# Kernel optimization log

Hardware: AMD Instinct MI355X
Metric: run time of the kernel (lower is better)

The kernel has to match this reference:

```python
import jax, jax.numpy as jnp
import numpy as np

B, SEQ, DIM = 4, 8192, 512
G = 32              # group_size: number of outer chunks (per source rearrange 'b (g n) d')
QK = 128            # query_key_dim
HD = QK // 4        # head_dim = 32 (used for softmax scale)
HEAD_D = 2 * HD     # per-head feature dim = 64 (h=2 heads over QK)
HID = DIM           # expansion_factor = 1.0
EPS = 1e-5


def _shift_seq(t):
    # F.pad(t, (0,0,1,-1)): prepend one zero row along axis=-2, drop last row
    pad = [(0, 0)] * (t.ndim - 2) + [(1, 0), (0, 0)]
    return jnp.pad(t, pad)[..., :-1, :]


def setup_inputs() -> dict:
    key = jax.random.key(0)
    ks = jax.random.split(key, 8)
    s = 0.02
    return {
        "x": jax.random.normal(ks[0], (B, SEQ, DIM), jnp.float32),
        "ln_g": jnp.ones((DIM,), jnp.float32),
        "ln_b": jnp.zeros((DIM,), jnp.float32),
        "w_qk": jax.random.normal(ks[1], (DIM, QK), jnp.float32) * s,
        "g4": jax.random.normal(ks[2], (4, QK), jnp.float32) * s,   # qk_offset_scale.gamma
        "b4": jnp.zeros((4, QK), jnp.float32),                       # qk_offset_scale.beta
        "g2": jax.random.normal(ks[3], (2, QK), jnp.float32) * s,   # shift_one_offset_scale.gamma
        "b2": jnp.zeros((2, QK), jnp.float32),
        "w_hidden": jax.random.normal(ks[4], (DIM, 2 * HID), jnp.float32) * s,
        "w_gate": jax.random.normal(ks[5], (DIM, HID), jnp.float32) * s,
        "w_out": jax.random.normal(ks[6], (5 * HID, DIM), jnp.float32) * s,
    }


def reference(x, ln_g, ln_b, w_qk, g4, b4, g2, b2, w_hidden, w_gate, w_out):
    b, seq, dim = x.shape
    n = seq // G  # tokens per chunk; seq chosen as multiple of G so padding = 0

    # LayerNorm
    mu = jnp.mean(x, axis=-1, keepdims=True)
    var = jnp.var(x, axis=-1, keepdims=True)
    xs = (x - mu) * jax.lax.rsqrt(var + EPS) * ln_g + ln_b

    # token shift of first half of channels (shift_tokens=True)
    half = dim // 2
    xs = jnp.concatenate([_shift_seq(xs[..., :half]), xs[..., half:]], axis=-1)

    qk = xs @ w_qk                                  # [b, seq, QK]
    qk_g = qk.reshape(b, G, n, QK)                  # 'b (g n) d -> b g n d', g outer
    qk_mean = qk_g.mean(axis=2)                     # [b, G, QK]

    # OffsetScale(heads=4) on per-chunk mean -> q_offset, k_offset, q_scale, k_scale
    offs = qk_mean[:, :, None, :] * g4 + b4         # [b, G, 4, QK]
    q_off, k_off, q_sc, k_sc = (offs[:, :, i, :] for i in range(4))

    q = qk_g * q_sc[:, :, None, :] + q_off[:, :, None, :]   # [b, G, n, QK]
    k = qk_g * k_sc[:, :, None, :] + k_off[:, :, None, :]

    # shift-by-one variants within each chunk, re-scaled + shift-one offsets
    q_s_off = qk_mean * g2[0] + b2[0]               # [b, G, QK]
    k_s_off = qk_mean * g2[1] + b2[1]
    qs = _shift_seq(q) * q_sc[:, :, None, :] + q_s_off[:, :, None, :]
    ks_ = _shift_seq(k) * k_sc[:, :, None, :] + k_s_off[:, :, None, :]

    def heads(t):  # [b,G,n,QK] -> [b,G,2,n,HEAD_D]
        return t.reshape(b, G, n, 2, HEAD_D).transpose(0, 1, 3, 2, 4)

    q_all = jnp.concatenate([heads(q), heads(qs)], axis=2)   # [b,G,4,n,64]
    k_all = jnp.concatenate([heads(k), heads(ks_)], axis=2)

    hg = xs @ w_hidden                              # [b, seq, 2*HID]
    hidden, gate = hg[..., :HID], hg[..., HID:]
    hidden_g = hidden.reshape(b, G, n, HID)

    sim = jnp.einsum('bghid,bghjd->bghij', q_all, k_all) * (HD ** -0.5)
    neg = -jnp.finfo(sim.dtype).max
    causal = jnp.triu(jnp.ones((n, n), dtype=bool), 1)  # applied unconditionally in source
    sim = jnp.where(causal, neg, sim)
    attn = jax.nn.softmax(sim, axis=-1)             # dropout=0 (eval)

    out = jnp.einsum('bghij,bgje->bghie', attn, hidden_g)   # [b,G,4,n,HID]
    gate_g = gate.reshape(b, G, n, HID)
    out = jax.nn.silu(out) * gate_g[:, :, None, :, :]
    out = out.transpose(0, 1, 3, 2, 4).reshape(b, seq, 4 * HID)  # 'b g h n e -> b (g n) (h e)'

    residual = jnp.concatenate([hidden, out], axis=-1)       # [b, seq, 5*HID]
    out = residual @ w_out                                   # [b, seq, dim]
    out = out * jax.nn.silu(xs @ w_gate)
    return out + xs
```

## Files before the change

### kernel.cpp

```cpp
#include <hip/hip_runtime.h>
#include <hip/hip_bf16.h>
#include <math.h>

#define BB 4
#define SEQ 8192
#define DIM 512
#define GG 32
#define NPG 256
#define QKD 128
#define HIDD 512

typedef unsigned short u16;
typedef unsigned int u32;

using s16x8 = __attribute__((ext_vector_type(8))) short;
using f32x4 = __attribute__((ext_vector_type(4))) float;

__device__ __forceinline__ float bf2f(u16 u) { return __uint_as_float(((u32)u) << 16); }
__device__ __forceinline__ u16 f2bf(float f) {
  u32 b = __float_as_uint(f);
  return (u16)((b + 0x7FFFu + ((b >> 16) & 1u)) >> 16);
}
__device__ __forceinline__ float silu_f(float x) { return x / (1.f + expf(-x)); }
__device__ __forceinline__ float4 fma4(float4 a, float4 b, float4 c) {
  return make_float4(a.x*b.x+c.x, a.y*b.y+c.y, a.z*b.z+c.z, a.w*b.w+c.w);
}
#define LD4(p, off) (*(const float4*)((p) + (off)))

__device__ __forceinline__ s16x8 aff8(s16x8 v, float4 s0, float4 s1, float4 o0, float4 o1) {
  union U { s16x8 x; u16 u[8]; };
  U in; in.x = v; U r;
  r.u[0] = f2bf(bf2f(in.u[0]) * s0.x + o0.x);
  r.u[1] = f2bf(bf2f(in.u[1]) * s0.y + o0.y);
  r.u[2] = f2bf(bf2f(in.u[2]) * s0.z + o0.z);
  r.u[3] = f2bf(bf2f(in.u[3]) * s0.w + o0.w);
  r.u[4] = f2bf(bf2f(in.u[4]) * s1.x + o1.x);
  r.u[5] = f2bf(bf2f(in.u[5]) * s1.y + o1.y);
  r.u[6] = f2bf(bf2f(in.u[6]) * s1.z + o1.z);
  r.u[7] = f2bf(bf2f(in.u[7]) * s1.w + o1.w);
  return r.x;
}
__device__ __forceinline__ s16x8 aff8s(s16x8 p, bool nz, float4 s0, float4 s1,
                                       float4 o0, float4 o1, float4 t0, float4 t1) {
  union U { s16x8 x; u16 u[8]; };
  U in; in.x = p; U r;
  float v;
  v = nz ? (bf2f(in.u[0]) * s0.x + o0.x) : 0.f; r.u[0] = f2bf(v * s0.x + t0.x);
  v = nz ? (bf2f(in.u[1]) * s0.y + o0.y) : 0.f; r.u[1] = f2bf(v * s0.y + t0.y);
  v = nz ? (bf2f(in.u[2]) * s0.z + o0.z) : 0.f; r.u[2] = f2bf(v * s0.z + t0.z);
  v = nz ? (bf2f(in.u[3]) * s0.w + o0.w) : 0.f; r.u[3] = f2bf(v * s0.w + t0.w);
  v = nz ? (bf2f(in.u[4]) * s1.x + o1.x) : 0.f; r.u[4] = f2bf(v * s1.x + t1.x);
  v = nz ? (bf2f(in.u[5]) * s1.y + o1.y) : 0.f; r.u[5] = f2bf(v * s1.y + t1.y);
  v = nz ? (bf2f(in.u[6]) * s1.z + o1.z) : 0.f; r.u[6] = f2bf(v * s1.z + t1.z);
  v = nz ? (bf2f(in.u[7]) * s1.w + o1.w) : 0.f; r.u[7] = f2bf(v * s1.w + t1.w);
  return r.x;
}

__global__ __launch_bounds__(256) void k_ln(const float* __restrict__ x,
    const float* __restrict__ lg, const float* __restrict__ lb, float* __restrict__ xs) {
  const int row = blockIdx.x;
  const int s = row & (SEQ - 1);
  const int t = threadIdx.x;
  const float* xr = x + (size_t)row * DIM;
  float v0 = xr[t], v1 = xr[t + 256];
  float sum = v0 + v1, sq = v0 * v0 + v1 * v1;
  #pragma unroll
  for (int o = 32; o; o >>= 1) { sum += __shfl_down(sum, o); sq += __shfl_down(sq, o); }
  __shared__ float sm[8];
  const int w = t >> 6;
  if ((t & 63) == 0) { sm[w] = sum; sm[4 + w] = sq; }
  __syncthreads();
  if (t == 0) {
    float S = sm[0] + sm[1] + sm[2] + sm[3];
    float Q = sm[4] + sm[5] + sm[6] + sm[7];
    float mu = S * (1.f / DIM);
    float var = Q * (1.f / DIM) - mu * mu;
    sm[0] = mu; sm[4] = rsqrtf(var + 1e-5f);
  }
  __syncthreads();
  const float mu = sm[0], rs = sm[4];
  float y0 = (v0 - mu) * rs * lg[t] + lb[t];
  float y1 = (v1 - mu) * rs * lg[t + 256] + lb[t + 256];
  xs[(size_t)row * DIM + t + 256] = y1;
  if (s + 1 < SEQ) xs[(size_t)(row + 1) * DIM + t] = y0;
  if (s == 0) xs[(size_t)row * DIM + t] = 0.f;
}

__global__ __launch_bounds__(256) void k_trw(const float* __restrict__ src, u16* __restrict__ dst,
    int N, int dstLD, int rowOff) {
  __shared__ u16 T[64][66];
  const int t = threadIdx.x;
  const int k0 = blockIdx.x * 64, n0 = blockIdx.y * 64;
  #pragma unroll
  for (int i = 0; i < 16; ++i) {
    int idx = t + 256 * i;
    int r = idx >> 6, c = idx & 63;
    T[c][r] = f2bf(src[(size_t)(k0 + r) * N + n0 + c]);
  }
  __syncthreads();
  #pragma unroll
  for (int i = 0; i < 16; ++i) {
    int idx = t + 256 * i;
    int r = idx >> 6, c = idx & 63;
    dst[(size_t)(rowOff + n0 + r) * dstLD + k0 + c] = T[r][c];
  }
}

__global__ __launch_bounds__(256) void k_trh(const u16* __restrict__ hidt, u16* __restrict__ hidr) {
  __shared__ u16 T[64][66];
  const int t = threadIdx.x;
  const int j0 = blockIdx.x * 64;
  const int e0 = blockIdx.y * 64;
  const int bg = blockIdx.z;
  #pragma unroll
  for (int i = 0; i < 16; ++i) {
    int idx = t + 256 * i; int r = idx >> 6, c = idx & 63;
    T[c][r] = hidt[((size_t)bg * 512 + e0 + r) * 256 + j0 + c];
  }
  __syncthreads();
  #pragma unroll
  for (int i = 0; i < 16; ++i) {
    int idx = t + 256 * i; int r = idx >> 6, c = idx & 63;
    hidr[((size_t)bg * 256 + j0 + r) * 512 + e0 + c] = T[r][c];
  }
}

__global__ __launch_bounds__(256, 2) void k_gemm1m(const float* __restrict__ xs,
    const u16* __restrict__ w1t, u16* __restrict__ qk, u16* __restrict__ hidt,
    u16* __restrict__ gate, u16* __restrict__ xg) {
  __shared__ u16 As[128][72];
  __shared__ u16 Bs[128][72];
  const int t = threadIdx.x;
  const int m0 = blockIdx.x * 128, n0 = blockIdx.y * 128;
  const int w = t >> 6, l = t & 63, lr = l & 15, lq = l >> 4;
  const int wr = (w >> 1) * 64, wc = (w & 1) * 64;
  const int sr = t >> 3;
  const int sk = (t & 7) * 8;
  f32x4 acc[4][4];
  #pragma unroll
  for (int i = 0; i < 4; ++i)
    #pragma unroll
    for (int j = 0; j < 4; ++j) acc[i][j] = (f32x4){0.f, 0.f, 0.f, 0.f};
  for (int k0 = 0; k0 < 512; k0 += 64) {
    s16x8 aS[4], bS[4];
    #pragma unroll
    for (int it = 0; it < 4; ++it) {
      const float* ap = xs + (size_t)(m0 + sr + it * 32) * 512 + k0 + sk;
      float4 f0 = *(const float4*)ap;
      float4 f1 = *(const float4*)(ap + 4);
      s16x8 v;
      v[0] = (short)f2bf(f0.x); v[1] = (short)f2bf(f0.y); v[2] = (short)f2bf(f0.z); v[3] = (short)f2bf(f0.w);
      v[4] = (short)f2bf(f1.x); v[5] = (short)f2bf(f1.y); v[6] = (short)f2bf(f1.z); v[7] = (short)f2bf(f1.w);
      aS[it] = v;
      bS[it] = *(const s16x8*)(w1t + (size_t)(n0 + sr + it * 32) * 512 + k0 + sk);
    }
    __syncthreads();
    #pragma unroll
    for (int it = 0; it < 4; ++it) {
      *(s16x8*)&As[sr + it * 32][sk] = aS[it];
      *(s16x8*)&Bs[sr + it * 32][sk] = bS[it];
    }
    __syncthreads();
    #pragma unroll
    for (int kk = 0; kk < 64; kk += 32) {
      s16x8 af[4], bf[4];
      #pragma unroll
      for (int fi = 0; fi < 4; ++fi) af[fi] = *(const s16x8*)&As[wr + fi * 16 + lr][kk + 8 * lq];
      #pragma unroll
      for (int fj = 0; fj < 4; ++fj) bf[fj] = *(const s16x8*)&Bs[wc + fj * 16 + lr][kk + 8 * lq];
      #pragma unroll
      for (int fi = 0; fi < 4; ++fi)
        #pragma unroll
        for (int fj = 0; fj < 4; ++fj)
          acc[fi][fj] = __builtin_amdgcn_mfma_f32_16x16x32_bf16(af[fi], bf[fj], acc[fi][fj], 0, 0, 0);
    }
  }
  if (n0 == 0) {
    #pragma unroll
    for (int fi = 0; fi < 4; ++fi)
      #pragma unroll
      for (int fj = 0; fj < 4; ++fj) {
        const int n = wc + fj * 16 + lr;
        const int mb = m0 + wr + fi * 16 + lq * 4;
        #pragma unroll
        for (int r = 0; r < 4; ++r)
          qk[(size_t)(mb + r) * QKD + n] = f2bf(acc[fi][fj][r]);
      }
  } else if (n0 < 640) {
    const int bg = m0 >> 8;
    #pragma unroll
    for (int fi = 0; fi < 4; ++fi)
      #pragma unroll
      for (int fj = 0; fj < 4; ++fj) {
        const int e = n0 - 128 + wc + fj * 16 + lr;
        const int j0 = (m0 & 255) + wr + fi * 16 + lq * 4;
        ushort4 pk;
        pk.x = f2bf(acc[fi][fj][0]); pk.y = f2bf(acc[fi][fj][1]);
        pk.z = f2bf(acc[fi][fj][2]); pk.w = f2bf(acc[fi][fj][3]);
        *(ushort4*)(hidt + ((size_t)bg * 512 + e) * 256 + j0) = pk;
      }
  } else if (n0 < 1152) {
    #pragma unroll
    for (int fi = 0; fi < 4; ++fi)
      #pragma unroll
      for (int fj = 0; fj < 4; ++fj) {
        const int n = n0 - 640 + wc + fj * 16 + lr;
        const int mb = m0 + wr + fi * 16 + lq * 4;
        #pragma unroll
        for (int r = 0; r < 4; ++r)
          gate[(size_t)(mb + r) * HIDD + n] = f2bf(acc[fi][fj][r]);
      }
  } else {
    #pragma unroll
    for (int fi = 0; fi < 4; ++fi)
      #pragma unroll
      for (int fj = 0; fj < 4; ++fj) {
        const int n = n0 - 1152 + wc + fj * 16 + lr;
        const int mb = m0 + wr + fi * 16 + lq * 4;
        #pragma unroll
        for (int r = 0; r < 4; ++r)
          xg[(size_t)(mb + r) * HIDD + n] = f2bf(silu_f(acc[fi][fj][r]));
      }
  }
}

__global__ __launch_bounds__(128) void k_qkmean(const u16* __restrict__ qk, float* __restrict__ qm) {
  const int bg = blockIdx.x;
  const int c = threadIdx.x;
  const u16* p = qk + (size_t)bg * NPG * QKD + c;
  float s = 0.f;
  for (int i = 0; i < NPG; ++i) s += bf2f(p[(size_t)i * QKD]);
  qm[(size_t)bg * QKD + c] = s * (1.f / NPG);
}

__global__ __launch_bounds__(256, 4) void k_attn(const u16* __restrict__ qk,
    const float* __restrict__ qm, const float* __restrict__ g4, const float* __restrict__ b4,
    const float* __restrict__ g2, const float* __restrict__ b2,
    const u16* __restrict__ hidt, const u16* __restrict__ gate, u16* __restrict__ out4) {
  __shared__ u16 Vs[64][264];
  const int t = threadIdx.x;
  const int l = t & 63;
  const int h = t >> 6;
  const int blk = blockIdx.x;
  const int iw = 15 - (blk & 15);
  const int bg = blk >> 4;
  const size_t grpRow = (size_t)bg * NPG;
  const int cbase = (h & 1) << 6;
  const int lr = l & 15, lq = l >> 4;
  const int i0 = iw * 16, ntmax = iw, jtmax = iw >> 1;
  const int irow = i0 + lr;
  const int cA = cbase + 8 * lq;
  const float* qmp = qm + bg * QKD;
  float4 qmA = LD4(qmp, cA),      qmB = LD4(qmp, cA + 4);
  float4 qmC = LD4(qmp, cA + 32), qmD = LD4(qmp, cA + 36);
  float4 qscA = fma4(qmA, LD4(g4, 2*QKD+cA),    LD4(b4, 2*QKD+cA));
  float4 qscB = fma4(qmB, LD4(g4, 2*QKD+cA+4),  LD4(b4, 2*QKD+cA+4));
  float4 qscC = fma4(qmC, LD4(g4, 2*QKD+cA+32), LD4(b4, 2*QKD+cA+32));
  float4 qscD = fma4(qmD, LD4(g4, 2*QKD+cA+36), LD4(b4, 2*QKD+cA+36));
  float4 qofA = fma4(qmA, LD4(g4, cA),      LD4(b4, cA));
  float4 qofB = fma4(qmB, LD4(g4, cA+4),    LD4(b4, cA+4));
  float4 qofC = fma4(qmC, LD4(g4, cA+32),   LD4(b4, cA+32));
  float4 qofD = fma4(qmD, LD4(g4, cA+36),   LD4(b4, cA+36));
  s16x8 qb0, qb1;
  {
    if (h < 2) {
      const u16* qrow = qk + (grpRow + irow) * QKD + cA;
      qb0 = aff8(*(const s16x8*)qrow,        qscA, qscB, qofA, qofB);
      qb1 = aff8(*(const s16x8*)(qrow + 32), qscC, qscD, qofC, qofD);
    } else {
      float4 qsoA = fma4(qmA, LD4(g2, cA),    LD4(b2, cA));
      float4 qsoB = fma4(qmB, LD4(g2, cA+4),  LD4(b2, cA+4));
      float4 qsoC = fma4(qmC, LD4(g2, cA+32), LD4(b2, cA+32));
      float4 qsoD = fma4(qmD, LD4(g2, cA+36), LD4(b2, cA+36));
      const u16* prow = qk + (grpRow + (irow ? irow - 1 : 0)) * QKD + cA;
      qb0 = aff8s(*(const s16x8*)prow,        irow > 0, qscA, qscB, qofA, qofB, qsoA, qsoB);
      qb1 = aff8s(*(const s16x8*)(prow + 32), irow > 0, qscC, qscD, qofC, qofD, qsoC, qsoD);
    }
  }
  float4 kscA = fma4(qmA, LD4(g4, 3*QKD+cA),    LD4(b4, 3*QKD+cA));
  float4 kscB = fma4(qmB, LD4(g4, 3*QKD+cA+4),  LD4(b4, 3*QKD+cA+4));
  float4 kscC = fma4(qmC, LD4(g4, 3*QKD+cA+32), LD4(b4, 3*QKD+cA+32));
  float4 kscD = fma4(qmD, LD4(g4, 3*QKD+cA+36), LD4(b4, 3*QKD+cA+36));
  float4 kofA = fma4(qmA, LD4(g4, QKD+cA),      LD4(b4, QKD+cA));
  float4 kofB = fma4(qmB, LD4(g4, QKD+cA+4),    LD4(b4, QKD+cA+4));
  float4 kofC = fma4(qmC, LD4(g4, QKD+cA+32),   LD4(b4, QKD+cA+32));
  float4 kofD = fma4(qmD, LD4(g4, QKD+cA+36),   LD4(b4, QKD+cA+36));
  f32x4 sfr[16];
  if (h < 2) {
    #pragma unroll
    for (int nt = 0; nt < 16; ++nt) if (nt <= ntmax) {
      const u16* kr = qk + (grpRow + nt * 16 + lr) * QKD + cA;
      s16x8 ka0 = aff8(*(const s16x8*)kr,        kscA, kscB, kofA, kofB);
      s16x8 ka1 = aff8(*(const s16x8*)(kr + 32), kscC, kscD, kofC, kofD);
      f32x4 c = {0.f, 0.f, 0.f, 0.f};
      c = __builtin_amdgcn_mfma_f32_16x16x32_bf16(ka0, qb0, c, 0, 0, 0);
      c = __builtin_amdgcn_mfma_f32_16x16x32_bf16(ka1, qb1, c, 0, 0, 0);
      sfr[nt] = c;
    }
  } else {
    float4 ksoA = fma4(qmA, LD4(g2, QKD+cA),    LD4(b2, QKD+cA));
    float4 ksoB = fma4(qmB, LD4(g2, QKD+cA+4),  LD4(b2, QKD+cA+4));
    float4 ksoC = fma4(qmC, LD4(g2, QKD+cA+32), LD4(b2, QKD+cA+32));
    float4 ksoD = fma4(qmD, LD4(g2, QKD+cA+36), LD4(b2, QKD+cA+36));
    #pragma unroll
    for (int nt = 0; nt < 16; ++nt) if (nt <= ntmax) {
      const int jrow = nt * 16 + lr;
      const u16* pr = qk + (grpRow + (jrow ? jrow - 1 : 0)) * QKD + cA;
      s16x8 ka0 = aff8s(*(const s16x8*)pr,        jrow > 0, kscA, kscB, kofA, kofB, ksoA, ksoB);
      s16x8 ka1 = aff8s(*(const s16x8*)(pr + 32), jrow > 0, kscC, kscD, kofC, kofD, ksoC, ksoD);
      f32x4 c = {0.f, 0.f, 0.f, 0.f};
      c = __builtin_amdgcn_mfma_f32_16x16x32_bf16(ka0, qb0, c, 0, 0, 0);
      c = __builtin_amdgcn_mfma_f32_16x16x32_bf16(ka1, qb1, c, 0, 0, 0);
      sfr[nt] = c;
    }
  }
  const float scl = 0.17677669529663687f;
  float mx = -3.4e38f;
  #pragma unroll
  for (int nt = 0; nt < 16; ++nt) if (nt <= ntmax) {
    #pragma unroll
    for (int r = 0; r < 4; ++r) {
      int j = nt * 16 + lq * 4 + r;
      if (j <= irow) mx = fmaxf(mx, sfr[nt][r] * scl);
    }
  }
  mx = fmaxf(mx, __shfl_xor(mx, 16));
  mx = fmaxf(mx, __shfl_xor(mx, 32));
  float sum = 0.f;
  u32 p01[16], p23[16];
  #pragma unroll
  for (int nt = 0; nt < 16; ++nt) { p01[nt] = 0u; p23[nt] = 0u; }
  #pragma unroll
  for (int nt = 0; nt < 16; ++nt) if (nt <= ntmax) {
    int j = nt * 16 + lq * 4;
    float e0 = (j + 0 <= irow) ? expf(sfr[nt][0] * scl - mx) : 0.f;
    float e1 = (j + 1 <= irow) ? expf(sfr[nt][1] * scl - mx) : 0.f;
    float e2 = (j + 2 <= irow) ? expf(sfr[nt][2] * scl - mx) : 0.f;
    float e3 = (j + 3 <= irow) ? expf(sfr[nt][3] * scl - mx) : 0.f;
    sum += (e0 + e1) + (e2 + e3);
    p01[nt] = (u32)f2bf(e0) | ((u32)f2bf(e1) << 16);
    p23[nt] = (u32)f2bf(e2) | ((u32)f2bf(e3) << 16);
  }
  sum += __shfl_xor(sum, 16);
  sum += __shfl_xor(sum, 32);
  const float inv = 1.f / sum;
  const int srcA = (l & 15) | ((l & 16) << 1);
  const int srcB = srcA + 16;
  const bool hi = (l >= 32);
  s16x8 bfr[8];
  #pragma unroll
  for (int jt = 0; jt < 8; ++jt) if (jt <= jtmax) {
    u32 a0 = __shfl((int)p01[2 * jt], srcA), a1 = __shfl((int)p23[2 * jt], srcA);
    u32 a2 = __shfl((int)p01[2 * jt], srcB), a3 = __shfl((int)p23[2 * jt], srcB);
    u32 b0 = __shfl((int)p01[2 * jt + 1], srcA), b1 = __shfl((int)p23[2 * jt + 1], srcA);
    u32 b2 = __shfl((int)p01[2 * jt + 1], srcB), b3 = __shfl((int)p23[2 * jt + 1], srcB);
    union { u32 u[4]; s16x8 v; } bb;
    bb.u[0] = hi ? b0 : a0; bb.u[1] = hi ? b1 : a1;
    bb.u[2] = hi ? b2 : a2; bb.u[3] = hi ? b3 : a3;
    bfr[jt] = bb.v;
  }
  const u16* vtb = hidt + (size_t)bg * (512 * 256);
  const size_t srow = grpRow + irow;
  const u16* gp = gate + srow * HIDD;
  u16* op = out4 + srow * 2048 + ((size_t)h << 9);
  for (int oct = 0; oct < 8; ++oct) {
    __syncthreads();
    const u16* src = vtb + (size_t)oct * 64 * 256;
    #pragma unroll
    for (int it = 0; it < 8; ++it) {
      int flat = it * 256 + t;
      int row = flat >> 5, col8 = (flat & 31) * 8;
      *(uint4*)&Vs[row][col8] = *(const uint4*)(src + (size_t)row * 256 + col8);
    }
    __syncthreads();
    f32x4 acc[4];
    #pragma unroll
    for (int ef = 0; ef < 4; ++ef) acc[ef] = (f32x4){0.f, 0.f, 0.f, 0.f};
    #pragma unroll
    for (int jt = 0; jt < 8; ++jt) if (jt <= jtmax) {
      __builtin_amdgcn_s_setprio(1);
      #pragma unroll
      for (int ef = 0; ef < 4; ++ef) {
        s16x8 va = *(const s16x8*)&Vs[ef * 16 + lr][jt * 32 + 8 * lq];
        acc[ef] = __builtin_amdgcn_mfma_f32_16x16x32_bf16(va, bfr[jt], acc[ef], 0, 0, 0);
      }
      __builtin_amdgcn_s_setprio(0);
    }
    #pragma unroll
    for (int ef = 0; ef < 4; ++ef) {
      const int e = oct * 64 + ef * 16 + lq * 4;
      ushort4 gu = *(const ushort4*)(gp + e);
      ushort4 ov;
      ov.x = f2bf(silu_f(acc[ef][0] * inv) * bf2f(gu.x));
      ov.y = f2bf(silu_f(acc[ef][1] * inv) * bf2f(gu.y));
      ov.z = f2bf(silu_f(acc[ef][2] * inv) * bf2f(gu.z));
      ov.w = f2bf(silu_f(acc[ef][3] * inv) * bf2f(gu.w));
      *(ushort4*)(op + e) = ov;
    }
  }
}

__global__ __launch_bounds__(256, 2) void k_gemm2m(const u16* __restrict__ hidr,
    const u16* __restrict__ out4, const u16* __restrict__ wt,
    const u16* __restrict__ xg, float* __restrict__ out) {
  __shared__ u16 As[128][72];
  __shared__ u16 Bs[128][72];
  const int t = threadIdx.x;
  const int m0 = blockIdx.x * 128, n0 = blockIdx.y * 128;
  const int w = t >> 6, l = t & 63, lr = l & 15, lq = l >> 4;
  const int wr = (w >> 1) * 64, wc = (w & 1) * 64;
  const int sr = t >> 3;
  const int sk = (t & 7) * 8;
  f32x4 acc[4][4];
  #pragma unroll
  for (int i = 0; i < 4; ++i)
    #pragma unroll
    for (int j = 0; j < 4; ++j) acc[i][j] = (f32x4){0.f, 0.f, 0.f, 0.f};
  for (int k0 = 0; k0 < 2560; k0 += 64) {
    const u16* abase; size_t ald; int koff;
    if (k0 < 512) { abase = hidr; ald = 512; koff = k0; }
    else          { abase = out4; ald = 2048; koff = k0 - 512; }
    s16x8 aS[4], bS[4];
    #pragma unroll
    for (int it = 0; it < 4; ++it) {
      aS[it] = *(const s16x8*)(abase + (size_t)(m0 + sr + it * 32) * ald + koff + sk);
      bS[it] = *(const s16x8*)(wt + (size_t)(n0 + sr + it * 32) * 2560 + k0 + sk);
    }
    __syncthreads();
    #pragma unroll
    for (int it = 0; it < 4; ++it) {
      *(s16x8*)&As[sr + it * 32][sk] = aS[it];
      *(s16x8*)&Bs[sr + it * 32][sk] = bS[it];
    }
    __syncthreads();
    #pragma unroll
    for (int kk = 0; kk < 64; kk += 32) {
      s16x8 af[4], bf[4];
      #pragma unroll
      for (int fi = 0; fi < 4; ++fi) af[fi] = *(const s16x8*)&As[wr + fi * 16 + lr][kk + 8 * lq];
      #pragma unroll
      for (int fj = 0; fj < 4; ++fj) bf[fj] = *(const s16x8*)&Bs[wc + fj * 16 + lr][kk + 8 * lq];
      #pragma unroll
      for (int fi = 0; fi < 4; ++fi)
        #pragma unroll
        for (int fj = 0; fj < 4; ++fj)
          acc[fi][fj] = __builtin_amdgcn_mfma_f32_16x16x32_bf16(af[fi], bf[fj], acc[fi][fj], 0, 0, 0);
    }
  }
  #pragma unroll
  for (int fi = 0; fi < 4; ++fi)
    #pragma unroll
    for (int fj = 0; fj < 4; ++fj) {
      const int n = n0 + wc + fj * 16 + lr;
      const int mb = m0 + wr + fi * 16 + lq * 4;
      #pragma unroll
      for (int r = 0; r < 4; ++r) {
        const size_t idx = (size_t)(mb + r) * DIM + n;
        out[idx] = acc[fi][fj][r] * bf2f(xg[idx]) + out[idx];
      }
    }
}

extern "C" void kernel_launch(void* const* d_in, const int* in_sizes, int n_in,
                              void* d_out, int out_size, void* d_ws, size_t ws_size,
                              hipStream_t stream) {
  const float* x        = (const float*)d_in[0];
  const float* lg       = (const float*)d_in[1];
  const float* lb       = (const float*)d_in[2];
  const float* w_qk     = (const float*)d_in[3];
  const float* g4       = (const float*)d_in[4];
  const float* b4       = (const float*)d_in[5];
  const float* g2       = (const float*)d_in[6];
  const float* b2       = (const float*)d_in[7];
  const float* w_hidden = (const float*)d_in[8];
  const float* w_gate   = (const float*)d_in[9];
  const float* w_out    = (const float*)d_in[10];
  if (ws_size < 247660544ull) return;
  char* ws = (char*)d_ws;
  float* QM   = (float*)(ws + 0);
  u16*   HIDT = (u16*)  (ws + 65536);
  u16*   GATE = (u16*)  (ws + 33619968);
  u16*   XG   = (u16*)  (ws + 67174400);
  u16*   QKb  = (u16*)  (ws + 100728832);
  u16*   W1T  = (u16*)  (ws + 109117440);
  u16*   WT   = (u16*)  (ws + 110821376);
  u16*   OUT4 = (u16*)  (ws + 113442816);
  u16*   HIDR = (u16*)  (ws + 33619968);
  float* XS   = (float*)d_out;
  float* OUT  = (float*)d_out;

  k_ln<<<BB * SEQ, 256, 0, stream>>>(x, lg, lb, XS);
  k_trw<<<dim3(8, 2),  256, 0, stream>>>(w_qk,     W1T, 128,  512,  0);
  k_trw<<<dim3(8, 16), 256, 0, stream>>>(w_hidden, W1T, 1024, 512,  128);
  k_trw<<<dim3(8, 8),  256, 0, stream>>>(w_gate,   W1T, 512,  512,  1152);
  k_trw<<<dim3(40, 8), 256, 0, stream>>>(w_out,    WT,  512,  2560, 0);
  k_gemm1m<<<dim3(256, 13), 256, 0, stream>>>(XS, W1T, QKb, HIDT, GATE, XG);
  k_qkmean<<<BB * GG, 128, 0, stream>>>(QKb, QM);
  k_attn<<<BB * GG * 16, 256, 0, stream>>>(QKb, QM, g4, b4, g2, b2, HIDT, GATE, OUT4);
  k_trh<<<dim3(4, 8, 128), 256, 0, stream>>>(HIDT, HIDR);
  k_gemm2m<<<dim3(256, 4), 256, 0, stream>>>(HIDR, OUT4, WT, XG, OUT);
}
```

Before: 474.9 us.

## Pair causal query tiles per attention block and fold shifted affine into one

Each attention block now handles two query tiles, a short one (pair) and a long one (15-pair), so causal work is balanced across blocks and the grid is halved. The shifted-head double affine is algebraically folded into a single scale/offset, with the zero-row case handled by a precomputed constant vector. Softmax and SiLU switch to fast __expf. The cost is that each block makes two sequential passes over V staging, and the fast exponential is slightly less precise.

```diff
diff --git a/kernel.cpp b/kernel.cpp
--- a/kernel.cpp
+++ b/kernel.cpp
@@ -22,8 +22,12 @@
   return (u16)((b + 0x7FFFu + ((b >> 16) & 1u)) >> 16);
 }
 __device__ __forceinline__ float silu_f(float x) { return x / (1.f + expf(-x)); }
+__device__ __forceinline__ float silu_fast(float x) { return x / (1.f + __expf(-x)); }
 __device__ __forceinline__ float4 fma4(float4 a, float4 b, float4 c) {
   return make_float4(a.x*b.x+c.x, a.y*b.y+c.y, a.z*b.z+c.z, a.w*b.w+c.w);
+}
+__device__ __forceinline__ float4 mul4(float4 a, float4 b) {
+  return make_float4(a.x*b.x, a.y*b.y, a.z*b.z, a.w*b.w);
 }
 #define LD4(p, off) (*(const float4*)((p) + (off)))
 
@@ -40,20 +44,11 @@
   r.u[7] = f2bf(bf2f(in.u[7]) * s1.w + o1.w);
   return r.x;
 }
-__device__ __forceinline__ s16x8 aff8s(s16x8 p, bool nz, float4 s0, float4 s1,
-                                       float4 o0, float4 o1, float4 t0, float4 t1) {
-  union U { s16x8 x; u16 u[8]; };
-  U in; in.x = p; U r;
-  float v;
-  v = nz ? (bf2f(in.u[0]) * s0.x + o0.x) : 0.f; r.u[0] = f2bf(v * s0.x + t0.x);
-  v = nz ? (bf2f(in.u[1]) * s0.y + o0.y) : 0.f; r.u[1] = f2bf(v * s0.y + t0.y);
-  v = nz ? (bf2f(in.u[2]) * s0.z + o0.z) : 0.f; r.u[2] = f2bf(v * s0.z + t0.z);
-  v = nz ? (bf2f(in.u[3]) * s0.w + o0.w) : 0.f; r.u[3] = f2bf(v * s0.w + t0.w);
-  v = nz ? (bf2f(in.u[4]) * s1.x + o1.x) : 0.f; r.u[4] = f2bf(v * s1.x + t1.x);
-  v = nz ? (bf2f(in.u[5]) * s1.y + o1.y) : 0.f; r.u[5] = f2bf(v * s1.y + t1.y);
-  v = nz ? (bf2f(in.u[6]) * s1.z + o1.z) : 0.f; r.u[6] = f2bf(v * s1.z + t1.z);
-  v = nz ? (bf2f(in.u[7]) * s1.w + o1.w) : 0.f; r.u[7] = f2bf(v * s1.w + t1.w);
-  return r.x;
+__device__ __forceinline__ s16x8 pack8(float4 a, float4 b) {
+  union { s16x8 v; u16 u[8]; } z;
+  z.u[0] = f2bf(a.x); z.u[1] = f2bf(a.y); z.u[2] = f2bf(a.z); z.u[3] = f2bf(a.w);
+  z.u[4] = f2bf(b.x); z.u[5] = f2bf(b.y); z.u[6] = f2bf(b.z); z.u[7] = f2bf(b.w);
+  return z.v;
 }
 
 __global__ __launch_bounds__(256) void k_ln(const float* __restrict__ x,
@@ -241,14 +236,13 @@
   const int t = threadIdx.x;
   const int l = t & 63;
   const int h = t >> 6;
+  const bool sh = (h >= 2);
   const int blk = blockIdx.x;
-  const int iw = 15 - (blk & 15);
-  const int bg = blk >> 4;
+  const int pair = blk & 7;
+  const int bg = blk >> 3;
   const size_t grpRow = (size_t)bg * NPG;
   const int cbase = (h & 1) << 6;
   const int lr = l & 15, lq = l >> 4;
-  const int i0 = iw * 16, ntmax = iw, jtmax = iw >> 1;
-  const int irow = i0 + lr;
   const int cA = cbase + 8 * lq;
   const float* qmp = qm + bg * QKD;
   float4 qmA = LD4(qmp, cA),      qmB = LD4(qmp, cA + 4);
@@ -261,22 +255,6 @@
   float4 qofB = fma4(qmB, LD4(g4, cA+4),    LD4(b4, cA+4));
   float4 qofC = fma4(qmC, LD4(g4, cA+32),   LD4(b4, cA+32));
   float4 qofD = fma4(qmD, LD4(g4, cA+36),   LD4(b4, cA+36));
-  s16x8 qb0, qb1;
-  {
-    if (h < 2) {
-      const u16* qrow = qk + (grpRow + irow) * QKD + cA;
-      qb0 = aff8(*(const s16x8*)qrow,        qscA, qscB, qofA, qofB);
-      qb1 = aff8(*(const s16x8*)(qrow + 32), qscC, qscD, qofC, qofD);
-    } else {
-      float4 qsoA = fma4(qmA, LD4(g2, cA),    LD4(b2, cA));
-      float4 qsoB = fma4(qmB, LD4(g2, cA+4),  LD4(b2, cA+4));
-      float4 qsoC = fma4(qmC, LD4(g2, cA+32), LD4(b2, cA+32));
-      float4 qsoD = fma4(qmD, LD4(g2, cA+36), LD4(b2, cA+36));
-      const u16* prow = qk + (grpRow + (irow ? irow - 1 : 0)) * QKD + cA;
-      qb0 = aff8s(*(const s16x8*)prow,        irow > 0, qscA, qscB, qofA, qofB, qsoA, qsoB);
-      qb1 = aff8s(*(const s16x8*)(prow + 32), irow > 0, qscC, qscD, qofC, qofD, qsoC, qsoD);
-    }
-  }
   float4 kscA = fma4(qmA, LD4(g4, 3*QKD+cA),    LD4(b4, 3*QKD+cA));
   float4 kscB = fma4(qmB, LD4(g4, 3*QKD+cA+4),  LD4(b4, 3*QKD+cA+4));
   float4 kscC = fma4(qmC, LD4(g4, 3*QKD+cA+32), LD4(b4, 3*QKD+cA+32));
@@ -285,117 +263,133 @@
   float4 kofB = fma4(qmB, LD4(g4, QKD+cA+4),    LD4(b4, QKD+cA+4));
   float4 kofC = fma4(qmC, LD4(g4, QKD+cA+32),   LD4(b4, QKD+cA+32));
   float4 kofD = fma4(qmD, LD4(g4, QKD+cA+36),   LD4(b4, QKD+cA+36));
-  f32x4 sfr[16];
-  if (h < 2) {
+  s16x8 qz0 = {0,0,0,0,0,0,0,0}, qz1 = qz0, kz0 = qz0, kz1 = qz0;
+  if (sh) {
+    float4 qsoA = fma4(qmA, LD4(g2, cA),    LD4(b2, cA));
+    float4 qsoB = fma4(qmB, LD4(g2, cA+4),  LD4(b2, cA+4));
+    float4 qsoC = fma4(qmC, LD4(g2, cA+32), LD4(b2, cA+32));
+    float4 qsoD = fma4(qmD, LD4(g2, cA+36), LD4(b2, cA+36));
+    float4 ksoA = fma4(qmA, LD4(g2, QKD+cA),    LD4(b2, QKD+cA));
+    float4 ksoB = fma4(qmB, LD4(g2, QKD+cA+4),  LD4(b2, QKD+cA+4));
+    float4 ksoC = fma4(qmC, LD4(g2, QKD+cA+32), LD4(b2, QKD+cA+32));
+    float4 ksoD = fma4(qmD, LD4(g2, QKD+cA+36), LD4(b2, QKD+cA+36));
+    qofA = fma4(qofA, qscA, qsoA); qofB = fma4(qofB, qscB, qsoB);
+    qofC = fma4(qofC, qscC, qsoC); qofD = fma4(qofD, qscD, qsoD);
+    qscA = mul4(qscA, qscA); qscB = mul4(qscB, qscB);
+    qscC = mul4(qscC, qscC); qscD = mul4(qscD, qscD);
+    kofA = fma4(kofA, kscA, ksoA); kofB = fma4(kofB, kscB, ksoB);
+    kofC = fma4(kofC, kscC, ksoC); kofD = fma4(kofD, kscD, ksoD);
+    kscA = mul4(kscA, kscA); kscB = mul4(kscB, kscB);
+    kscC = mul4(kscC, kscC); kscD = mul4(kscD, kscD);
+    qz0 = pack8(qsoA, qsoB); qz1 = pack8(qsoC, qsoD);
+    kz0 = pack8(ksoA, ksoB); kz1 = pack8(ksoC, ksoD);
+  }
+  const u16* vtb = hidt + (size_t)bg * (512 * 256);
+  const float scl = 0.17677669529663687f;
+  for (int tl = 0; tl < 2; ++tl) {
+    const int iw = tl ? (15 - pair) : pair;
+    const int i0 = iw * 16, ntmax = iw, jtmax = iw >> 1;
+    const int irow = i0 + lr;
+    const int qsrc = sh ? (irow ? irow - 1 : 0) : irow;
+    const u16* qrow = qk + (grpRow + qsrc) * QKD + cA;
+    s16x8 qb0 = aff8(*(const s16x8*)qrow,        qscA, qscB, qofA, qofB);
+    s16x8 qb1 = aff8(*(const s16x8*)(qrow + 32), qscC, qscD, qofC, qofD);
+    if (sh && irow == 0) { qb0 = qz0; qb1 = qz1; }
+    f32x4 sfr[16];
     #pragma unroll
     for (int nt = 0; nt < 16; ++nt) if (nt <= ntmax) {
-      const u16* kr = qk + (grpRow + nt * 16 + lr) * QKD + cA;
+      const int jr = nt * 16 + lr;
+      const int ksrc = sh ? (jr ? jr - 1 : 0) : jr;
+      const u16* kr = qk + (grpRow + ksrc) * QKD + cA;
       s16x8 ka0 = aff8(*(const s16x8*)kr,        kscA, kscB, kofA, kofB);
       s16x8 ka1 = aff8(*(const s16x8*)(kr + 32), kscC, kscD, kofC, kofD);
+      if (sh && jr == 0) { ka0 = kz0; ka1 = kz1; }
       f32x4 c = {0.f, 0.f, 0.f, 0.f};
       c = __builtin_amdgcn_mfma_f32_16x16x32_bf16(ka0, qb0, c, 0, 0, 0);
       c = __builtin_amdgcn_mfma_f32_16x16x32_bf16(ka1, qb1, c, 0, 0, 0);
       sfr[nt] = c;
     }
-  } else {
-    float4 ksoA = fma4(qmA, LD4(g2, QKD+cA),    LD4(b2, QKD+cA));
-    float4 ksoB = fma4(qmB, LD4(g2, QKD+cA+4),  LD4(b2, QKD+cA+4));
-    float4 ksoC = fma4(qmC, LD4(g2, QKD+cA+32), LD4(b2, QKD+cA+32));
-    float4 ksoD = fma4(qmD, LD4(g2, QKD+cA+36), LD4(b2, QKD+cA+36));
+    float mx = -3.4e38f;
     #pragma unroll
     for (int nt = 0; nt < 16; ++nt) if (nt <= ntmax) {
-      const int jrow = nt * 16 + lr;
-      const u16* pr = qk + (grpRow + (jrow ? jrow - 1 : 0)) * QKD + cA;
-      s16x8 ka0 = aff8s(*(const s16x8*)pr,        jrow > 0, kscA, kscB, kofA, kofB, ksoA, ksoB);
-      s16x8 ka1 = aff8s(*(const s16x8*)(pr + 32), jrow > 0, kscC, kscD, kofC, kofD, ksoC, ksoD);
-      f32x4 c = {0.f, 0.f, 0.f, 0.f};
-      c = __builtin_amdgcn_mfma_f32_16x16x32_bf16(ka0, qb0, c, 0, 0, 0);
-      c = __builtin_amdgcn_mfma_f32_16x16x32_bf16(ka1, qb1, c, 0, 0, 0);
-      sfr[nt] = c;
-    }
-  }
-  const float scl = 0.17677669529663687f;
-  float mx = -3.4e38f;
-  #pragma unroll
-  for (int nt = 0; nt < 16; ++nt) if (nt <= ntmax) {
-    #pragma unroll
-    for (int r = 0; r < 4; ++r) {
-      int j = nt * 16 + lq * 4 + r;
-      if (j <= irow) mx = fmaxf(mx, sfr[nt][r] * scl);
-    }
-  }
-  mx = fmaxf(mx, __shfl_xor(mx, 16));
-  mx = fmaxf(mx, __shfl_xor(mx, 32));
-  float sum = 0.f;
-  u32 p01[16], p23[16];
-  #pragma unroll
-  for (int nt = 0; nt < 16; ++nt) { p01[nt] = 0u; p23[nt] = 0u; }
-  #pragma unroll
-  for (int nt = 0; nt < 16; ++nt) if (nt <= ntmax) {
-    int j = nt * 16 + lq * 4;
-    float e0 = (j + 0 <= irow) ? expf(sfr[nt][0] * scl - mx) : 0.f;
-    float e1 = (j + 1 <= irow) ? expf(sfr[nt][1] * scl - mx) : 0.f;
-    float e2 = (j + 2 <= irow) ? expf(sfr[nt][2] * scl - mx) : 0.f;
-    float e3 = (j + 3 <= irow) ? expf(sfr[nt][3] * scl - mx) : 0.f;
-    sum += (e0 + e1) + (e2 + e3);
-    p01[nt] = (u32)f2bf(e0) | ((u32)f2bf(e1) << 16);
-    p23[nt] = (u32)f2bf(e2) | ((u32)f2bf(e3) << 16);
-  }
-  sum += __shfl_xor(sum, 16);
-  sum += __shfl_xor(sum, 32);
-  const float inv = 1.f / sum;
-  const int srcA = (l & 15) | ((l & 16) << 1);
-  const int srcB = srcA + 16;
-  const bool hi = (l >= 32);
-  s16x8 bfr[8];
-  #pragma unroll
-  for (int jt = 0; jt < 8; ++jt) if (jt <= jtmax) {
-    u32 a0 = __shfl((int)p01[2 * jt], srcA), a1 = __shfl((int)p23[2 * jt], srcA);
-    u32 a2 = __shfl((int)p01[2 * jt], srcB), a3 = __shfl((int)p23[2 * jt], srcB);
-    u32 b0 = __shfl((int)p01[2 * jt + 1], srcA), b1 = __shfl((int)p23[2 * jt + 1], srcA);
-    u32 b2 = __shfl((int)p01[2 * jt + 1], srcB), b3 = __shfl((int)p23[2 * jt + 1], srcB);
-    union { u32 u[4]; s16x8 v; } bb;
-    bb.u[0] = hi ? b0 : a0; bb.u[1] = hi ? b1 : a1;
-    bb.u[2] = hi ? b2 : a2; bb.u[3] = hi ? b3 : a3;
-    bfr[jt] = bb.v;
-  }
-  const u16* vtb = hidt + (size_t)bg * (512 * 256);
-  const size_t srow = grpRow + irow;
-  const u16* gp = gate + srow * HIDD;
-  u16* op = out4 + srow * 2048 + ((size_t)h << 9);
-  for (int oct = 0; oct < 8; ++oct) {
-    __syncthreads();
-    const u16* src = vtb + (size_t)oct * 64 * 256;
-    #pragma unroll
-    for (int it = 0; it < 8; ++it) {
-      int flat = it * 256 + t;
-      int row = flat >> 5, col8 = (flat & 31) * 8;
-      *(uint4*)&Vs[row][col8] = *(const uint4*)(src + (size_t)row * 256 + col8);
-    }
-    __syncthreads();
-    f32x4 acc[4];
-    #pragma unroll
-    for (int ef = 0; ef < 4; ++ef) acc[ef] = (f32x4){0.f, 0.f, 0.f, 0.f};
+      #pragma unroll
+      for (int r = 0; r < 4; ++r) {
+        int j = nt * 16 + lq * 4 + r;
+        if (j <= irow) mx = fmaxf(mx, sfr[nt][r] * scl);
+      }
+    }
+    mx = fmaxf(mx, __shfl_xor(mx, 16));
+    mx = fmaxf(mx, __shfl_xor(mx, 32));
+    float sum = 0.f;
+    u32 p01[16], p23[16];
+    #pragma unroll
+    for (int nt = 0; nt < 16; ++nt) { p01[nt] = 0u; p23[nt] = 0u; }
+    #pragma unroll
+    for (int nt = 0; nt < 16; ++nt) if (nt <= ntmax) {
+      int j = nt * 16 + lq * 4;
+      float e0 = (j + 0 <= irow) ? __expf(sfr[nt][0] * scl - mx) : 0.f;
+      float e1 = (j + 1 <= irow) ? __expf(sfr[nt][1] * scl - mx) : 0.f;
+      float e2 = (j + 2 <= irow) ? __expf(sfr[nt][2] * scl - mx) : 0.f;
+      float e3 = (j + 3 <= irow) ? __expf(sfr[nt][3] * scl - mx) : 0.f;
+      sum += (e0 + e1) + (e2 + e3);
+      p01[nt] = (u32)f2bf(e0) | ((u32)f2bf(e1) << 16);
+      p23[nt] = (u32)f2bf(e2) | ((u32)f2bf(e3) << 16);
+    }
+    sum += __shfl_xor(sum, 16);
+    sum += __shfl_xor(sum, 32);
+    const float inv = 1.f / sum;
+    const int srcA = (l & 15) | ((l & 16) << 1);
+    const int srcB = srcA + 16;
+    const bool hi = (l >= 32);
+    s16x8 bfr[8];
     #pragma unroll
     for (int jt = 0; jt < 8; ++jt) if (jt <= jtmax) {
-      __builtin_amdgcn_s_setprio(1);
+      u32 a0 = __shfl((int)p01[2 * jt], srcA), a1 = __shfl((int)p23[2 * jt], srcA);
+      u32 a2 = __shfl((int)p01[2 * jt], srcB), a3 = __shfl((int)p23[2 * jt], srcB);
+      u32 b0 = __shfl((int)p01[2 * jt + 1], srcA), b1 = __shfl((int)p23[2 * jt + 1], srcA);
+      u32 b2 = __shfl((int)p01[2 * jt + 1], srcB), b3 = __shfl((int)p23[2 * jt + 1], srcB);
+      union { u32 u[4]; s16x8 v; } bb;
+      bb.u[0] = hi ? b0 : a0; bb.u[1] = hi ? b1 : a1;
+      bb.u[2] = hi ? b2 : a2; bb.u[3] = hi ? b3 : a3;
+      bfr[jt] = bb.v;
+    }
+    const size_t srow = grpRow + irow;
+    const u16* gp = gate + srow * HIDD;
+    u16* op = out4 + srow * 2048 + ((size_t)h << 9);
+    for (int oct = 0; oct < 8; ++oct) {
+      __syncthreads();
+      const u16* src = vtb + (size_t)oct * 64 * 256;
+      #pragma unroll
+      for (int it = 0; it < 8; ++it) {
+        int flat = it * 256 + t;
+        int row = flat >> 5, col8 = (flat & 31) * 8;
+        *(uint4*)&Vs[row][col8] = *(const uint4*)(src + (size_t)row * 256 + col8);
+      }
+      __syncthreads();
+      f32x4 acc[4];
+      #pragma unroll
+      for (int ef = 0; ef < 4; ++ef) acc[ef] = (f32x4){0.f, 0.f, 0.f, 0.f};
+      #pragma unroll
+      for (int jt = 0; jt < 8; ++jt) if (jt <= jtmax) {
+        __builtin_amdgcn_s_setprio(1);
+        #pragma unroll
+        for (int ef = 0; ef < 4; ++ef) {
+          s16x8 va = *(const s16x8*)&Vs[ef * 16 + lr][jt * 32 + 8 * lq];
+          acc[ef] = __builtin_amdgcn_mfma_f32_16x16x32_bf16(va, bfr[jt], acc[ef], 0, 0, 0);
+        }
+        __builtin_amdgcn_s_setprio(0);
+      }
       #pragma unroll
       for (int ef = 0; ef < 4; ++ef) {
-        s16x8 va = *(const s16x8*)&Vs[ef * 16 + lr][jt * 32 + 8 * lq];
-        acc[ef] = __builtin_amdgcn_mfma_f32_16x16x32_bf16(va, bfr[jt], acc[ef], 0, 0, 0);
-      }
-      __builtin_amdgcn_s_setprio(0);
-    }
-    #pragma unroll
-    for (int ef = 0; ef < 4; ++ef) {
-      const int e = oct * 64 + ef * 16 + lq * 4;
-      ushort4 gu = *(const ushort4*)(gp + e);
-      ushort4 ov;
-      ov.x = f2bf(silu_f(acc[ef][0] * inv) * bf2f(gu.x));
-      ov.y = f2bf(silu_f(acc[ef][1] * inv) * bf2f(gu.y));
-      ov.z = f2bf(silu_f(acc[ef][2] * inv) * bf2f(gu.z));
-      ov.w = f2bf(silu_f(acc[ef][3] * inv) * bf2f(gu.w));
-      *(ushort4*)(op + e) = ov;
+        const int e = oct * 64 + ef * 16 + lq * 4;
+        ushort4 gu = *(const ushort4*)(gp + e);
+        ushort4 ov;
+        ov.x = f2bf(silu_fast(acc[ef][0] * inv) * bf2f(gu.x));
+        ov.y = f2bf(silu_fast(acc[ef][1] * inv) * bf2f(gu.y));
+        ov.z = f2bf(silu_fast(acc[ef][2] * inv) * bf2f(gu.z));
+        ov.w = f2bf(silu_fast(acc[ef][3] * inv) * bf2f(gu.w));
+        *(ushort4*)(op + e) = ov;
+      }
     }
   }
 }
@@ -496,7 +490,7 @@
   k_trw<<<dim3(40, 8), 256, 0, stream>>>(w_out,    WT,  512,  2560, 0);
   k_gemm1m<<<dim3(256, 13), 256, 0, stream>>>(XS, W1T, QKb, HIDT, GATE, XG);
   k_qkmean<<<BB * GG, 128, 0, stream>>>(QKb, QM);
-  k_attn<<<BB * GG * 16, 256, 0, stream>>>(QKb, QM, g4, b4, g2, b2, HIDT, GATE, OUT4);
+  k_attn<<<BB * GG * 8, 256, 0, stream>>>(QKb, QM, g4, b4, g2, b2, HIDT, GATE, OUT4);
   k_trh<<<dim3(4, 8, 128), 256, 0, stream>>>(HIDT, HIDR);
   k_gemm2m<<<dim3(256, 4), 256, 0, stream>>>(HIDR, OUT4, WT, XG, OUT);
 }
```

Measured after the change: 593.1 us. +24.9%, slower.
